# Optimization experiments

Measured on AMD Instinct MI355X. Metric: run time of the kernel, lower is better.

The kernel has to match this reference:

```python
import jax, jax.numpy as jnp
import numpy as np
from itertools import product as _prod

B = 2          # batch size
NPB = 4096     # voxels per batch
C = 384        # input_dim
H = 8          # num_heads
OUT = 32       # output_dim (seg classes)
SPATIAL = (32, 256, 256)
POOL_R = np.array([1, 2, 2, 2])    # [1]+query_gs_ratio
COMP_R = np.array([1, 16, 16, 16])  # [1]+compress_ratio


def _coords():
    rng = np.random.default_rng(0)
    rows = []
    for b in range(B):
        cand = np.stack([rng.integers(0, s, 4 * NPB) for s in SPATIAL], 1)
        cand = np.unique(cand, axis=0)
        sel = cand[rng.permutation(len(cand))[:NPB]]
        rows.append(np.concatenate([np.full((NPB, 1), b, np.int64), sel], 1))
    return np.concatenate(rows).astype(np.int32)


def setup_inputs() -> dict:
    idx = _coords()                     # [N,4] unique (b,z,y,x)
    N = idx.shape[0]
    pool_u, pool_inv = np.unique(idx // POOL_R, axis=0, return_inverse=True)
    emb_u, emb_inv = np.unique(idx // COMP_R, axis=0, return_inverse=True)
    # submanifold 3x3x3 neighbor table (same batch), -1 = missing
    lut = {tuple(r): i for i, r in enumerate(idx.tolist())}
    nbr = np.full((N, 27), -1, np.int32)
    rows = idx.tolist()
    for k, (dz, dy, dx) in enumerate(_prod((-1, 0, 1), repeat=3)):
        for i, (b, z, y, x) in enumerate(rows):
            nbr[i, k] = lut.get((b, z + dz, y + dy, x + dx), -1)
    key = jax.random.key(0)
    ks = jax.random.split(key, 12)
    g = lambda k, shp, s: jax.random.normal(k, shp, jnp.float32) * s
    s = 1.0 / float(np.sqrt(C))
    return dict(
        feats=g(ks[0], (N, C), 1.0),
        W_pool=g(ks[1], (C, C), s), b_pool=jnp.zeros((C,), jnp.float32),
        W_emb=g(ks[2], (C, C), s), b_emb=jnp.zeros((C,), jnp.float32),
        Wq=g(ks[3], (C, C), s), bq=jnp.zeros((C,), jnp.float32),
        Wk=g(ks[4], (C, C), s), bk=jnp.zeros((C,), jnp.float32),
        Wv=g(ks[5], (C, C), s), bv=jnp.zeros((C,), jnp.float32),
        Wo=g(ks[6], (C, C), s), bo=jnp.zeros((C,), jnp.float32),
        W_conv=g(ks[7], (27, C, OUT), 1.0 / float(np.sqrt(27 * C))),
        b_conv=jnp.zeros((OUT,), jnp.float32),
        pool_inv=jnp.asarray(pool_inv, jnp.int32),
        pool_coords=jnp.asarray(pool_u, jnp.int32),
        emb_inv=jnp.asarray(emb_inv, jnp.int32),
        emb_coords=jnp.asarray(emb_u, jnp.int32),
        nbr_idx=jnp.asarray(nbr),
        batch_size=B,
    )


def _sine_pe(xyz, d_pos):
    # xyz: [n,3] normalized to [0,1]; PositionEmbeddingCoordsSine (3detr-style)
    cdim = d_pos // xyz.shape[1]
    dim_t = 10000.0 ** (2.0 * (jnp.arange(cdim) // 2).astype(jnp.float32) / cdim)
    emb = (xyz * (2.0 * jnp.pi))[:, :, None] / dim_t          # [n,3,cdim]
    pe = jnp.stack([jnp.sin(emb[..., 0::2]), jnp.cos(emb[..., 1::2])], -1)
    return pe.reshape(xyz.shape[0], -1)                        # [n,d_pos]


def reference(feats, W_pool, b_pool, W_emb, b_emb, Wq, bq, Wk, bk, Wv, bv,
              Wo, bo, W_conv, b_conv, pool_inv, pool_coords, emb_inv,
              emb_coords, nbr_idx, batch_size):
    Mp, Me, Cc = pool_coords.shape[0], emb_coords.shape[0], feats.shape[1]
    hd = Cc // H
    # query path: linear + scatter_max over pool cells
    pool_f = jax.ops.segment_max(feats @ W_pool + b_pool, pool_inv, num_segments=Mp)
    # kv path: linear + scatter_max over compressed cells (coords of argmax rows
    # within a cell all equal the unique cell coord, so mean == unique coord)
    emb_f = jax.ops.segment_max(feats @ W_emb + b_emb, emb_inv, num_segments=Me)
    # per-batch min/max-normalized sine positional encoding on concat(emb,pool)
    emb_xyz = emb_coords[:, 1:].astype(jnp.float32)
    pool_xyz = pool_coords[:, 1:].astype(jnp.float32)
    all_xyz = jnp.concatenate([emb_xyz, pool_xyz], 0)
    bids = jnp.concatenate([emb_coords[:, 0], pool_coords[:, 0]], 0)
    mins = jax.ops.segment_min(all_xyz, bids, num_segments=batch_size)
    maxs = jax.ops.segment_max(all_xyz, bids, num_segments=batch_size)
    norm = (all_xyz - mins[bids]) / (maxs[bids] - mins[bids] + 1e-6)
    pe = _sine_pe(norm, Cc)
    emb_f = emb_f + pe[:Me]
    pool_f = pool_f + pe[Me:]
    # multi-head cross-attention, masked to same-batch pairs
    q = (pool_f @ Wq + bq).reshape(Mp, H, hd)
    k = (emb_f @ Wk + bk).reshape(Me, H, hd)
    v = (emb_f @ Wv + bv).reshape(Me, H, hd)
    scores = jnp.einsum('phd,ehd->hpe', q, k) / jnp.sqrt(jnp.float32(hd))
    same_b = pool_coords[:, 0][None, :, None] == emb_coords[:, 0][None, None, :]
    attn = jax.nn.softmax(jnp.where(same_b, scores, -1e9), axis=-1)
    o = jnp.einsum('hpe,ehd->phd', attn, v).reshape(Mp, Cc) @ Wo + bo
    # broadcast back to voxels + residual
    new_f = feats + o[pool_inv]
    # SubMConv3d seg head: gather 27 neighbors, contract with kernel
    valid = (nbr_idx >= 0)[:, :, None]
    gathered = jnp.where(valid, new_f[jnp.maximum(nbr_idx, 0)], 0.0)  # [N,27,C]
    logits = jnp.einsum('nkc,kco->no', gathered, W_conv) + b_conv
    return logits
```

## Files before the change

kernel.cpp:

```cpp
#include <hip/hip_runtime.h>
#include <hip/hip_bf16.h>
#include <math.h>

#define CDIM 384
#define NHEAD 8
#define HD 48
#define OUTD 32
#define MAXB 16
#define CONVK 10368

typedef __bf16 bf16x8 __attribute__((ext_vector_type(8)));
typedef float f32x4 __attribute__((ext_vector_type(4)));

__device__ __forceinline__ f32x4 mfma16(bf16x8 a, bf16x8 b, f32x4 c) {
  return __builtin_amdgcn_mfma_f32_16x16x32_bf16(a, b, c, 0, 0, 0);
}
__device__ __forceinline__ bf16x8 zero8() {
  bf16x8 z = {(__bf16)0.f, (__bf16)0.f, (__bf16)0.f, (__bf16)0.f,
              (__bf16)0.f, (__bf16)0.f, (__bf16)0.f, (__bf16)0.f};
  return z;
}

__device__ __forceinline__ unsigned enc_f(float f) {
  unsigned u = __float_as_uint(f);
  return (u & 0x80000000u) ? ~u : (u | 0x80000000u);
}
__device__ __forceinline__ float dec_f(unsigned u) {
  unsigned v = (u & 0x80000000u) ? (u ^ 0x80000000u) : ~u;
  return __uint_as_float(v);
}

__global__ void init_small_kernel(int* smin, int* smax, int* eb) {
  int t = threadIdx.x;
  if (t < MAXB * 3) { smin[t] = 0x7fffffff; smax[t] = (int)0x80000000; }
  if (t <= MAXB) eb[t] = 0;
}

__global__ void minmax_kernel(const int* __restrict__ ec, int Me,
                              const int* __restrict__ pc, int Mp,
                              int* smin, int* smax) {
  __shared__ int lmin[MAXB * 3], lmax[MAXB * 3];
  int t = threadIdx.x;
  if (t < MAXB * 3) { lmin[t] = 0x7fffffff; lmax[t] = (int)0x80000000; }
  __syncthreads();
  int i = blockIdx.x * blockDim.x + t;
  int tot = Me + Mp;
  if (i < tot) {
    const int* r = (i < Me) ? (ec + 4 * i) : (pc + 4 * (i - Me));
    int b = r[0];
    #pragma unroll
    for (int d = 0; d < 3; ++d) {
      atomicMin(&lmin[b * 3 + d], r[1 + d]);
      atomicMax(&lmax[b * 3 + d], r[1 + d]);
    }
  }
  __syncthreads();
  if (t < MAXB * 3) {
    if (lmin[t] != 0x7fffffff) atomicMin(&smin[t], lmin[t]);
    if (lmax[t] != (int)0x80000000) atomicMax(&smax[t], lmax[t]);
  }
}

__global__ void ebound_kernel(const int* __restrict__ ec, int Me,
                              const int* __restrict__ bsz, int* eb) {
  int e = blockIdx.x * blockDim.x + threadIdx.x;
  if (e == 0) { eb[0] = 0; eb[bsz[0]] = Me; }
  if (e > 0 && e < Me) {
    int b0 = ec[4 * (e - 1)], b1 = ec[4 * e];
    for (int bb = b0 + 1; bb <= b1; ++bb) eb[bb] = e;
  }
}

__global__ __launch_bounds__(256) void prep_kernel(
    const float* __restrict__ feats, __hip_bfloat16* __restrict__ feats16, int N,
    const float* __restrict__ W_pool, const float* __restrict__ W_emb,
    const float* __restrict__ Wk, const float* __restrict__ Wv,
    const float* __restrict__ Wq, const float* __restrict__ Wo,
    __hip_bfloat16* __restrict__ Wt_pe, __hip_bfloat16* __restrict__ Wt_kv,
    __hip_bfloat16* __restrict__ Wt_q, __hip_bfloat16* __restrict__ Wt_o,
    const float* __restrict__ Wc, __hip_bfloat16* __restrict__ Wct,
    __hip_bfloat16* __restrict__ vt, int Mepad,
    int nbF, int nbW, int nbC) {
  int b = blockIdx.x;
  int t = threadIdx.x;
  if (b < nbF) {
    int v = b * 256 + t;
    if (v < N * 48) {
      float4 a0 = *reinterpret_cast<const float4*>(feats + (size_t)v * 8);
      float4 a1 = *reinterpret_cast<const float4*>(feats + (size_t)v * 8 + 4);
      __hip_bfloat16 tmp[8] = {
        __float2bfloat16(a0.x), __float2bfloat16(a0.y), __float2bfloat16(a0.z), __float2bfloat16(a0.w),
        __float2bfloat16(a1.x), __float2bfloat16(a1.y), __float2bfloat16(a1.z), __float2bfloat16(a1.w)};
      *reinterpret_cast<bf16x8*>(feats16 + (size_t)v * 8) = *reinterpret_cast<const bf16x8*>(tmp);
    }
    return;
  }
  b -= nbF;
  if (b < 6 * nbW) {
    int m = b / nbW;
    int v = (b - m * nbW) * 256 + t;
    if (v >= CDIM * 48) return;
    const float* src;
    __hip_bfloat16* dst;
    switch (m) {
      case 0: src = W_pool; dst = Wt_pe; break;
      case 1: src = W_emb;  dst = Wt_pe + (size_t)CDIM * CDIM; break;
      case 2: src = Wk;     dst = Wt_kv; break;
      case 3: src = Wv;     dst = Wt_kv + (size_t)CDIM * CDIM; break;
      case 4: src = Wq;     dst = Wt_q; break;
      default: src = Wo;    dst = Wt_o; break;
    }
    int n = v / 48, k8 = (v - n * 48) * 8;
    __hip_bfloat16 tmp[8];
    #pragma unroll
    for (int u = 0; u < 8; ++u) tmp[u] = __float2bfloat16(src[(size_t)(k8 + u) * CDIM + n]);
    *reinterpret_cast<bf16x8*>(dst + (size_t)n * CDIM + k8) = *reinterpret_cast<const bf16x8*>(tmp);
    return;
  }
  b -= 6 * nbW;
  if (b < nbC) {
    int v = b * 256 + t;
    if (v >= OUTD * (CONVK / 8)) return;
    int n = v / (CONVK / 8), k8 = (v - n * (CONVK / 8)) * 8;
    __hip_bfloat16 tmp[8];
    #pragma unroll
    for (int u = 0; u < 8; ++u) tmp[u] = __float2bfloat16(Wc[(size_t)(k8 + u) * OUTD + n]);
    *reinterpret_cast<bf16x8*>(Wct + (size_t)n * CONVK + k8) = *reinterpret_cast<const bf16x8*>(tmp);
    return;
  }
  b -= nbC;
  {
    int v = b * 256 + t;
    if (v < NHEAD * Mepad) {
      int h = v / Mepad, e = v - h * Mepad;
      vt[(size_t)(h * 64 + HD) * Mepad + e] = __float2bfloat16(1.0f);
    }
  }
}

__global__ void pe_kernel(const unsigned* __restrict__ encP, const unsigned* __restrict__ encE,
                          __hip_bfloat16* __restrict__ pool16, __hip_bfloat16* __restrict__ emb16,
                          const int* __restrict__ pc, int Mp,
                          const int* __restrict__ ec, int Me,
                          const int* __restrict__ smin, const int* __restrict__ smax) {
  int gid = blockIdx.x * blockDim.x + threadIdx.x;
  int total = (Mp + Me) * CDIM;
  if (gid >= total) return;
  int row = gid / CDIM, c = gid - row * CDIM;
  const int* coords;
  const unsigned* src;
  __hip_bfloat16* dst;
  int lrow;
  if (row < Me) { lrow = row; coords = ec + 4 * row; src = encE; dst = emb16; }
  else { lrow = row - Me; coords = pc + 4 * lrow; src = encP; dst = pool16; }
  int b = coords[0];
  int dim = c >> 7;
  int i = c & 127;
  int j = i >> 1;
  float x = (float)coords[1 + dim];
  float mn = (float)smin[b * 3 + dim];
  float mx = (float)smax[b * 3 + dim];
  float nrm = (x - mn) / (mx - mn + 1e-6f);
  float freq = exp2f(-(float)j * 0.20762050593046014f);
  float arg = nrm * 6.283185307179586f * freq;
  float pe = (i & 1) ? cosf(arg) : sinf(arg);
  float val = dec_f(src[(size_t)lrow * CDIM + c]) + pe;
  dst[(size_t)lrow * CDIM + c] = __float2bfloat16(val);
}

template <int EPI>
__global__ __launch_bounds__(256) void mgemm_kernel(
    const __hip_bfloat16* __restrict__ A, int M,
    const __hip_bfloat16* __restrict__ Wt,
    const float* __restrict__ bias0, const float* __restrict__ bias1,
    void* __restrict__ d0, void* __restrict__ d1,
    const int* __restrict__ inv0, const int* __restrict__ inv1,
    int Mepad) {
  __shared__ __align__(16) __hip_bfloat16 As[128][72];
  __shared__ __align__(16) __hip_bfloat16 Bs[64][72];
  const int m0 = blockIdx.x * 128;
  const int n0 = blockIdx.y * 64;
  const int t = threadIdx.x;
  const int lane = t & 63, w = t >> 6;
  const int wr = w >> 1, wc = w & 1;
  const int lq = lane & 15, lg = lane >> 4;

  f32x4 acc[4][2];
  #pragma unroll
  for (int i = 0; i < 4; ++i) {
    acc[i][0] = (f32x4){0.f, 0.f, 0.f, 0.f};
    acc[i][1] = (f32x4){0.f, 0.f, 0.f, 0.f};
  }
  const int arow = t >> 3;
  const int acol = (t & 7) * 8;

  for (int k0 = 0; k0 < CDIM; k0 += 64) {
    #pragma unroll
    for (int i = 0; i < 4; ++i) {
      int r = arow + i * 32;
      int gr = m0 + r;
      bf16x8 val = zero8();
      if (gr < M) val = *reinterpret_cast<const bf16x8*>(A + (size_t)gr * CDIM + k0 + acol);
      *reinterpret_cast<bf16x8*>(&As[r][acol]) = val;
    }
    #pragma unroll
    for (int i = 0; i < 2; ++i) {
      int r = arow + i * 32;
      bf16x8 val = *reinterpret_cast<const bf16x8*>(Wt + (size_t)(n0 + r) * CDIM + k0 + acol);
      *reinterpret_cast<bf16x8*>(&Bs[r][acol]) = val;
    }
    __syncthreads();
    #pragma unroll
    for (int ks = 0; ks < 2; ++ks) {
      bf16x8 af[4], bfv[2];
      #pragma unroll
      for (int fm = 0; fm < 4; ++fm)
        af[fm] = *reinterpret_cast<const bf16x8*>(&As[wr * 64 + fm * 16 + lq][ks * 32 + lg * 8]);
      #pragma unroll
      for (int fn = 0; fn < 2; ++fn)
        bfv[fn] = *reinterpret_cast<const bf16x8*>(&Bs[wc * 32 + fn * 16 + lq][ks * 32 + lg * 8]);
      #pragma unroll
      for (int fm = 0; fm < 4; ++fm)
        #pragma unroll
        for (int fn = 0; fn < 2; ++fn)
          acc[fm][fn] = mfma16(af[fm], bfv[fn], acc[fm][fn]);
    }
    __syncthreads();
  }

  const bool sec = (n0 >= CDIM);
  const int nb = n0 - (sec ? CDIM : 0) + wc * 32;
  const int nA = nb + lq, nB = nb + 16 + lq;

  if (EPI == 0) {
    const float* bias = sec ? bias1 : bias0;
    unsigned* dst = (unsigned*)(sec ? d1 : d0);
    const int* inv = sec ? inv1 : inv0;
    float bA = bias[nA], bB = bias[nB];
    #pragma unroll
    for (int fm = 0; fm < 4; ++fm)
      #pragma unroll
      for (int j = 0; j < 4; ++j) {
        int r = m0 + wr * 64 + fm * 16 + lg * 4 + j;
        if (r < M) {
          int seg = inv[r];
          atomicMax(&dst[(size_t)seg * CDIM + nA], enc_f(acc[fm][0][j] + bA));
          atomicMax(&dst[(size_t)seg * CDIM + nB], enc_f(acc[fm][1][j] + bB));
        }
      }
  } else if (EPI == 1) {
    float bA = bias0[nA], bB = bias0[nB];
    float* dst = (float*)d0;
    #pragma unroll
    for (int fm = 0; fm < 4; ++fm)
      #pragma unroll
      for (int j = 0; j < 4; ++j) {
        int r = m0 + wr * 64 + fm * 16 + lg * 4 + j;
        if (r < M) {
          dst[(size_t)r * CDIM + nA] = acc[fm][0][j] + bA;
          dst[(size_t)r * CDIM + nB] = acc[fm][1][j] + bB;
        }
      }
  } else if (EPI == 2) {
    const float scale = 0.14433756729740643f;
    float bA = bias0[nA], bB = bias0[nB];
    int hA = nA / HD, dA = nA - hA * HD;
    int hB = nB / HD, dB = nB - hB * HD;
    __hip_bfloat16* dst = (__hip_bfloat16*)d0;
    #pragma unroll
    for (int fm = 0; fm < 4; ++fm)
      #pragma unroll
      for (int j = 0; j < 4; ++j) {
        int r = m0 + wr * 64 + fm * 16 + lg * 4 + j;
        if (r < M) {
          dst[(size_t)r * 512 + hA * 64 + dA] = __float2bfloat16((acc[fm][0][j] + bA) * scale);
          dst[(size_t)r * 512 + hB * 64 + dB] = __float2bfloat16((acc[fm][1][j] + bB) * scale);
        }
      }
  } else {
    if (!sec) {
      float bA = bias0[nA], bB = bias0[nB];
      int hA = nA / HD, dA = nA - hA * HD;
      int hB = nB / HD, dB = nB - hB * HD;
      __hip_bfloat16* dst = (__hip_bfloat16*)d0;
      #pragma unroll
      for (int fm = 0; fm < 4; ++fm)
        #pragma unroll
        for (int j = 0; j < 4; ++j) {
          int r = m0 + wr * 64 + fm * 16 + lg * 4 + j;
          if (r < M) {
            dst[(size_t)r * 512 + hA * 64 + dA] = __float2bfloat16(acc[fm][0][j] + bA);
            dst[(size_t)r * 512 + hB * 64 + dB] = __float2bfloat16(acc[fm][1][j] + bB);
          }
        }
    } else {
      float bA = bias1[nA], bB = bias1[nB];
      int hA = nA / HD, dA = nA - hA * HD;
      int hB = nB / HD, dB = nB - hB * HD;
      __hip_bfloat16* dst = (__hip_bfloat16*)d1;
      #pragma unroll
      for (int fm = 0; fm < 4; ++fm)
        #pragma unroll
        for (int j = 0; j < 4; ++j) {
          int r = m0 + wr * 64 + fm * 16 + lg * 4 + j;
          if (r < M) {
            dst[(size_t)(hA * 64 + dA) * Mepad + r] = __float2bfloat16(acc[fm][0][j] + bA);
            dst[(size_t)(hB * 64 + dB) * Mepad + r] = __float2bfloat16(acc[fm][1][j] + bB);
          }
        }
    }
  }
}

__global__ __launch_bounds__(256) void attn_mfma_kernel(
    const __hip_bfloat16* __restrict__ qb, const __hip_bfloat16* __restrict__ kb,
    const __hip_bfloat16* __restrict__ vt, int Mepad,
    const int* __restrict__ pc, const int* __restrict__ eb,
    int Mp, int Me, __hip_bfloat16* __restrict__ ob) {
  __shared__ __align__(16) __hip_bfloat16 Ks[64][72];
  __shared__ __align__(16) __hip_bfloat16 Vs[64][72];
  __shared__ __align__(16) __hip_bfloat16 pl[4][16][72];
  __shared__ int s_lo[4], s_hi[4];
  const int h = blockIdx.y;
  const int t = threadIdx.x;
  const int wv = t >> 6, lane = t & 63;
  const int lq = lane & 15, lg = lane >> 4;
  const int q0 = blockIdx.x * 64 + wv * 16;

  int lo[4], hi[4];
  #pragma unroll
  for (int r = 0; r < 4; ++r) {
    int q = q0 + lg * 4 + r;
    if (q < Mp) { int b = pc[4 * q]; lo[r] = eb[b]; hi[r] = eb[b + 1]; }
    else { lo[r] = 0x7fffffff; hi[r] = 0; }
  }
  int wlo = min(min(lo[0], lo[1]), min(lo[2], lo[3]));
  int whi = max(max(hi[0], hi[1]), max(hi[2], hi[3]));
  #pragma unroll
  for (int off = 1; off < 64; off <<= 1) {
    wlo = min(wlo, __shfl_xor(wlo, off));
    whi = max(whi, __shfl_xor(whi, off));
  }
  if (lane == 0) { s_lo[wv] = wlo; s_hi[wv] = whi; }
  __syncthreads();
  int blo = min(min(s_lo[0], s_lo[1]), min(s_lo[2], s_lo[3]));
  int bhi = max(max(s_hi[0], s_hi[1]), max(s_hi[2], s_hi[3]));
  blo &= ~63;

  int qrow = min(q0 + lq, Mp - 1);
  const __hip_bfloat16* qp = qb + (size_t)qrow * 512 + h * 64 + lg * 8;
  bf16x8 aq0 = *reinterpret_cast<const bf16x8*>(qp);
  bf16x8 aq1 = *reinterpret_cast<const bf16x8*>(qp + 32);

  const int str = t >> 2;
  const int stc = (t & 3) * 16;
  const __hip_bfloat16* vrow = vt + (size_t)(h * 64 + str) * Mepad + stc;

  f32x4 zero = {0.f, 0.f, 0.f, 0.f};
  f32x4 oacc[4];
  oacc[0] = zero; oacc[1] = zero; oacc[2] = zero; oacc[3] = zero;

  bf16x8 k0, k1, v0, v1;
  auto load_tile = [&](int e0) {
    int er = e0 + str;
    k0 = zero8(); k1 = zero8();
    if (er < Me) {
      const __hip_bfloat16* kp = kb + (size_t)er * 512 + h * 64 + stc;
      k0 = *reinterpret_cast<const bf16x8*>(kp);
      k1 = *reinterpret_cast<const bf16x8*>(kp + 8);
    }
    v0 = *reinterpret_cast<const bf16x8*>(vrow + e0);
    v1 = *reinterpret_cast<const bf16x8*>(vrow + e0 + 8);
  };
  load_tile(blo);

  for (int e0 = blo; e0 < bhi; e0 += 64) {
    __syncthreads();
    *reinterpret_cast<bf16x8*>(&Ks[str][stc]) = k0;
    *reinterpret_cast<bf16x8*>(&Ks[str][stc + 8]) = k1;
    *reinterpret_cast<bf16x8*>(&Vs[str][stc]) = v0;
    *reinterpret_cast<bf16x8*>(&Vs[str][stc + 8]) = v1;
    __syncthreads();
    if (e0 + 64 < bhi) load_tile(e0 + 64);

    f32x4 sf[4];
    #pragma unroll
    for (int s = 0; s < 4; ++s) {
      bf16x8 bk0 = *reinterpret_cast<const bf16x8*>(&Ks[s * 16 + lq][lg * 8]);
      bf16x8 bk1 = *reinterpret_cast<const bf16x8*>(&Ks[s * 16 + lq][32 + lg * 8]);
      f32x4 z = zero;
      z = mfma16(aq0, bk0, z);
      z = mfma16(aq1, bk1, z);
      sf[s] = z;
    }
    #pragma unroll
    for (int s = 0; s < 4; ++s) {
      int e = e0 + s * 16 + lq;
      #pragma unroll
      for (int r = 0; r < 4; ++r) {
        bool m = (e >= lo[r]) && (e < hi[r]);
        float p = m ? __expf(sf[s][r]) : 0.f;
        pl[wv][lg * 4 + r][s * 16 + lq] = __float2bfloat16(p);
      }
    }
    asm volatile("s_waitcnt lgkmcnt(0)" ::: "memory");
    __builtin_amdgcn_sched_barrier(0);
    #pragma unroll
    for (int ks = 0; ks < 2; ++ks) {
      bf16x8 ap = *reinterpret_cast<const bf16x8*>(&pl[wv][lq][ks * 32 + lg * 8]);
      #pragma unroll
      for (int dt = 0; dt < 4; ++dt) {
        bf16x8 bv = *reinterpret_cast<const bf16x8*>(&Vs[dt * 16 + lq][ks * 32 + lg * 8]);
        oacc[dt] = mfma16(ap, bv, oacc[dt]);
      }
    }
  }

  #pragma unroll
  for (int r = 0; r < 4; ++r) {
    float l = __shfl(oacc[3][r], (lane & 48));
    int q = q0 + lg * 4 + r;
    if (q < Mp && l > 0.f) {
      float inv = 1.0f / l;
      __hip_bfloat16* op = ob + (size_t)q * CDIM + h * HD;
      op[lq]      = __float2bfloat16(oacc[0][r] * inv);
      op[16 + lq] = __float2bfloat16(oacc[1][r] * inv);
      op[32 + lq] = __float2bfloat16(oacc[2][r] * inv);
    }
  }
}

__global__ void newf16_kernel(const float* __restrict__ feats, const float* __restrict__ o2,
                              const int* __restrict__ pinv, __hip_bfloat16* __restrict__ nf,
                              int N) {
  int v = blockIdx.x * 256 + threadIdx.x;
  if (v >= N * 48) return;
  int n = v / 48, c8 = (v - n * 48) * 8;
  const float* fp = feats + (size_t)n * CDIM + c8;
  const float* op = o2 + (size_t)pinv[n] * CDIM + c8;
  float4 a0 = *reinterpret_cast<const float4*>(fp);
  float4 a1 = *reinterpret_cast<const float4*>(fp + 4);
  float4 b0 = *reinterpret_cast<const float4*>(op);
  float4 b1 = *reinterpret_cast<const float4*>(op + 4);
  __hip_bfloat16 tmp[8] = {
    __float2bfloat16(a0.x + b0.x), __float2bfloat16(a0.y + b0.y),
    __float2bfloat16(a0.z + b0.z), __float2bfloat16(a0.w + b0.w),
    __float2bfloat16(a1.x + b1.x), __float2bfloat16(a1.y + b1.y),
    __float2bfloat16(a1.z + b1.z), __float2bfloat16(a1.w + b1.w)};
  *reinterpret_cast<bf16x8*>(nf + (size_t)v * 8) = *reinterpret_cast<const bf16x8*>(tmp);
}

__global__ __launch_bounds__(256) void mconv_kernel(
    const __hip_bfloat16* __restrict__ nf, const int* __restrict__ nbr,
    const __hip_bfloat16* __restrict__ Wct, float* __restrict__ outp, int N) {
  __shared__ __align__(16) __hip_bfloat16 As[128][72];
  __shared__ __align__(16) __hip_bfloat16 Bs[32][72];
  __shared__ int jrow[128];
  const int n0 = blockIdx.x * 128;
  const int kg = blockIdx.y;
  const int t = threadIdx.x;
  const int lane = t & 63, w = t >> 6;
  const int lq = lane & 15, lg = lane >> 4;
  f32x4 acc[2][2];
  acc[0][0] = (f32x4){0.f,0.f,0.f,0.f}; acc[0][1] = acc[0][0];
  acc[1][0] = acc[0][0]; acc[1][1] = acc[0][0];
  const int arow = t >> 3, acol = (t & 7) * 8;

  for (int kk = kg * 3; kk < kg * 3 + 3; ++kk) {
    __syncthreads();
    if (t < 128) {
      int n = n0 + t;
      jrow[t] = (n < N) ? nbr[(size_t)n * 27 + kk] : -1;
    }
    __syncthreads();
    for (int c0 = 0; c0 < CDIM; c0 += 64) {
      #pragma unroll
      for (int i = 0; i < 4; ++i) {
        int r = arow + i * 32;
        int j = jrow[r];
        bf16x8 val = zero8();
        if (j >= 0) val = *reinterpret_cast<const bf16x8*>(nf + (size_t)j * CDIM + c0 + acol);
        *reinterpret_cast<bf16x8*>(&As[r][acol]) = val;
      }
      {
        int r = t >> 3;
        bf16x8 val = *reinterpret_cast<const bf16x8*>(Wct + (size_t)r * CONVK + kk * CDIM + c0 + acol);
        *reinterpret_cast<bf16x8*>(&Bs[r][acol]) = val;
      }
      __syncthreads();
      #pragma unroll
      for (int ks = 0; ks < 2; ++ks) {
        bf16x8 af[2], bfv[2];
        #pragma unroll
        for (int fm = 0; fm < 2; ++fm)
          af[fm] = *reinterpret_cast<const bf16x8*>(&As[w * 32 + fm * 16 + lq][ks * 32 + lg * 8]);
        #pragma unroll
        for (int fn = 0; fn < 2; ++fn)
          bfv[fn] = *reinterpret_cast<const bf16x8*>(&Bs[fn * 16 + lq][ks * 32 + lg * 8]);
        #pragma unroll
        for (int fm = 0; fm < 2; ++fm)
          #pragma unroll
          for (int fn = 0; fn < 2; ++fn)
            acc[fm][fn] = mfma16(af[fm], bfv[fn], acc[fm][fn]);
      }
      __syncthreads();
    }
  }
  #pragma unroll
  for (int fm = 0; fm < 2; ++fm)
    #pragma unroll
    for (int j = 0; j < 4; ++j) {
      int r = n0 + w * 32 + fm * 16 + lg * 4 + j;
      if (r < N) {
        #pragma unroll
        for (int fn = 0; fn < 2; ++fn)
          outp[((size_t)kg * N + r) * OUTD + fn * 16 + lq] = acc[fm][fn][j];
      }
    }
}

__global__ void conv_reduce_kernel(const float* __restrict__ outp,
                                   const float* __restrict__ bc,
                                   float* __restrict__ out, int N) {
  int v = blockIdx.x * 256 + threadIdx.x;
  if (v >= N * OUTD) return;
  int oo = v & (OUTD - 1);
  float s = bc[oo];
  #pragma unroll
  for (int kg = 0; kg < 9; ++kg) s += outp[(size_t)kg * N * OUTD + v];
  out[v] = s;
}

extern "C" void kernel_launch(void* const* d_in, const int* in_sizes, int n_in,
                              void* d_out, int out_size, void* d_ws, size_t ws_size,
                              hipStream_t stream) {
  const float* feats  = (const float*)d_in[0];
  const float* W_pool = (const float*)d_in[1];
  const float* b_pool = (const float*)d_in[2];
  const float* W_emb  = (const float*)d_in[3];
  const float* b_emb  = (const float*)d_in[4];
  const float* Wq = (const float*)d_in[5];  const float* bq = (const float*)d_in[6];
  const float* Wk = (const float*)d_in[7];  const float* bk = (const float*)d_in[8];
  const float* Wv = (const float*)d_in[9];  const float* bv = (const float*)d_in[10];
  const float* Wo = (const float*)d_in[11]; const float* bo = (const float*)d_in[12];
  const float* Wc = (const float*)d_in[13]; const float* bc = (const float*)d_in[14];
  const int* pool_inv    = (const int*)d_in[15];
  const int* pool_coords = (const int*)d_in[16];
  const int* emb_inv     = (const int*)d_in[17];
  const int* emb_coords  = (const int*)d_in[18];
  const int* nbr         = (const int*)d_in[19];
  const int* bsz         = (const int*)d_in[20];
  int N  = in_sizes[0] / CDIM;
  int Mp = in_sizes[16] / 4;
  int Me = in_sizes[18] / 4;
  int Mepad = ((Me >> 6) + 2) << 6;

  char* wsb = (char*)d_ws;
  size_t off = 0;
  auto alloc = [&](size_t bytes) { void* p = wsb + off; off += (bytes + 255) & ~(size_t)255; return p; };
  unsigned* encA = (unsigned*)alloc((size_t)Mp * CDIM * 4);
  unsigned* encB = (unsigned*)alloc((size_t)Me * CDIM * 4);
  __hip_bfloat16* vt = (__hip_bfloat16*)alloc((size_t)512 * Mepad * 2);
  size_t zspan1 = off;
  __hip_bfloat16* pool16  = (__hip_bfloat16*)alloc((size_t)Mp * CDIM * 2);
  __hip_bfloat16* emb16   = (__hip_bfloat16*)alloc((size_t)Me * CDIM * 2);
  __hip_bfloat16* feats16 = (__hip_bfloat16*)alloc((size_t)N * CDIM * 2);
  float* o2 = (float*)alloc((size_t)Mp * CDIM * 4 > (size_t)9 * N * OUTD * 4
                                ? (size_t)Mp * CDIM * 4 : (size_t)9 * N * OUTD * 4);
  __hip_bfloat16* Wt_pe = (__hip_bfloat16*)alloc((size_t)768 * CDIM * 2);
  __hip_bfloat16* Wt_kv = (__hip_bfloat16*)alloc((size_t)768 * CDIM * 2);
  __hip_bfloat16* Wt_q  = (__hip_bfloat16*)alloc((size_t)CDIM * CDIM * 2);
  __hip_bfloat16* Wt_o  = (__hip_bfloat16*)alloc((size_t)CDIM * CDIM * 2);
  __hip_bfloat16* Wct   = (__hip_bfloat16*)alloc((size_t)OUTD * CONVK * 2);
  int* smin = (int*)alloc(MAXB * 3 * 4);
  int* smax = (int*)alloc(MAXB * 3 * 4);
  int* eb   = (int*)alloc((MAXB + 1) * 4);

  __hip_bfloat16* q16  = (__hip_bfloat16*)encA;
  __hip_bfloat16* k16  = (__hip_bfloat16*)encB;
  __hip_bfloat16* ob16 = pool16;
  __hip_bfloat16* newf16 = feats16;
  float* outp = o2;

  hipMemsetAsync(wsb, 0, zspan1, stream);
  init_small_kernel<<<1, 64, 0, stream>>>(smin, smax, eb);
  {
    int tot = Me + Mp;
    minmax_kernel<<<(tot + 255) / 256, 256, 0, stream>>>(emb_coords, Me, pool_coords, Mp, smin, smax);
    ebound_kernel<<<(Me + 255) / 256, 256, 0, stream>>>(emb_coords, Me, bsz, eb);
  }
  int nbF = (N * 48 + 255) / 256;
  int nbW = (CDIM * 48 + 255) / 256;
  int nbC = (OUTD * (CONVK / 8) + 255) / 256;
  int nbV = (NHEAD * Mepad + 255) / 256;
  prep_kernel<<<nbF + 6 * nbW + nbC + nbV, 256, 0, stream>>>(
      feats, feats16, N, W_pool, W_emb, Wk, Wv, Wq, Wo,
      Wt_pe, Wt_kv, Wt_q, Wt_o, Wc, Wct, vt, Mepad, nbF, nbW, nbC);

  mgemm_kernel<0><<<dim3((N + 127) / 128, 12), 256, 0, stream>>>(
      feats16, N, Wt_pe, b_pool, b_emb, encA, encB, pool_inv, emb_inv, 0);
  pe_kernel<<<((Mp + Me) * CDIM + 255) / 256, 256, 0, stream>>>(
      encA, encB, pool16, emb16, pool_coords, Mp, emb_coords, Me, smin, smax);

  hipMemsetAsync(encA, 0, (size_t)((char*)encB - (char*)encA) + (size_t)Me * 1024, stream);

  mgemm_kernel<2><<<dim3((Mp + 127) / 128, 6), 256, 0, stream>>>(
      pool16, Mp, Wt_q, bq, nullptr, q16, nullptr, nullptr, nullptr, 0);
  mgemm_kernel<3><<<dim3((Me + 127) / 128, 12), 256, 0, stream>>>(
      emb16, Me, Wt_kv, bk, bv, k16, vt, nullptr, nullptr, Mepad);

  attn_mfma_kernel<<<dim3((Mp + 63) / 64, NHEAD), 256, 0, stream>>>(
      q16, k16, vt, Mepad, pool_coords, eb, Mp, Me, ob16);

  mgemm_kernel<1><<<dim3((Mp + 127) / 128, 6), 256, 0, stream>>>(
      ob16, Mp, Wt_o, bo, nullptr, o2, nullptr, nullptr, nullptr, 0);

  newf16_kernel<<<(N * 48 + 255) / 256, 256, 0, stream>>>(feats, o2, pool_inv, newf16, N);

  mconv_kernel<<<dim3((N + 127) / 128, 9), 256, 0, stream>>>(newf16, nbr, Wct, outp, N);
  conv_reduce_kernel<<<(N * OUTD + 255) / 256, 256, 0, stream>>>(outp, bc, (float*)d_out, N);
}
```

Measured before the change: 194.6 us.

## Fuse setup kernels into prep, coalesce transposes, pre-reduce segment-max atomics, skip mask in attention

Folds the min/max and batch-boundary kernels into the prep kernel and replaces the init kernel with memsets, cutting launch count. Changes weight-transpose indexing so adjacent threads read adjacent source columns for coalescing. The pooling epilogue merges consecutive rows with the same segment before issuing atomicMax, and attention folds log2e into the Q scale to use exp2f, skipping mask checks for interior tiles. Correctness relies on memset byte patterns producing the right min/max sentinels and on eb not needing zero init.

```diff
diff --git a/kernel.cpp b/kernel.cpp
--- a/kernel.cpp
+++ b/kernel.cpp
@@ -28,47 +28,6 @@
 __device__ __forceinline__ float dec_f(unsigned u) {
   unsigned v = (u & 0x80000000u) ? (u ^ 0x80000000u) : ~u;
   return __uint_as_float(v);
-}
-
-__global__ void init_small_kernel(int* smin, int* smax, int* eb) {
-  int t = threadIdx.x;
-  if (t < MAXB * 3) { smin[t] = 0x7fffffff; smax[t] = (int)0x80000000; }
-  if (t <= MAXB) eb[t] = 0;
-}
-
-__global__ void minmax_kernel(const int* __restrict__ ec, int Me,
-                              const int* __restrict__ pc, int Mp,
-                              int* smin, int* smax) {
-  __shared__ int lmin[MAXB * 3], lmax[MAXB * 3];
-  int t = threadIdx.x;
-  if (t < MAXB * 3) { lmin[t] = 0x7fffffff; lmax[t] = (int)0x80000000; }
-  __syncthreads();
-  int i = blockIdx.x * blockDim.x + t;
-  int tot = Me + Mp;
-  if (i < tot) {
-    const int* r = (i < Me) ? (ec + 4 * i) : (pc + 4 * (i - Me));
-    int b = r[0];
-    #pragma unroll
-    for (int d = 0; d < 3; ++d) {
-      atomicMin(&lmin[b * 3 + d], r[1 + d]);
-      atomicMax(&lmax[b * 3 + d], r[1 + d]);
-    }
-  }
-  __syncthreads();
-  if (t < MAXB * 3) {
-    if (lmin[t] != 0x7fffffff) atomicMin(&smin[t], lmin[t]);
-    if (lmax[t] != (int)0x80000000) atomicMax(&smax[t], lmax[t]);
-  }
-}
-
-__global__ void ebound_kernel(const int* __restrict__ ec, int Me,
-                              const int* __restrict__ bsz, int* eb) {
-  int e = blockIdx.x * blockDim.x + threadIdx.x;
-  if (e == 0) { eb[0] = 0; eb[bsz[0]] = Me; }
-  if (e > 0 && e < Me) {
-    int b0 = ec[4 * (e - 1)], b1 = ec[4 * e];
-    for (int bb = b0 + 1; bb <= b1; ++bb) eb[bb] = e;
-  }
 }
 
 __global__ __launch_bounds__(256) void prep_kernel(
@@ -80,7 +39,10 @@
     __hip_bfloat16* __restrict__ Wt_q, __hip_bfloat16* __restrict__ Wt_o,
     const float* __restrict__ Wc, __hip_bfloat16* __restrict__ Wct,
     __hip_bfloat16* __restrict__ vt, int Mepad,
-    int nbF, int nbW, int nbC) {
+    const int* __restrict__ ec, const int* __restrict__ pc, int Mp, int Me,
+    const int* __restrict__ bsz, int* smin, int* smax, int* ebv,
+    int nbF, int nbW, int nbC, int nbV, int nbM) {
+  __shared__ int lmin[MAXB * 3], lmax[MAXB * 3];
   int b = blockIdx.x;
   int t = threadIdx.x;
   if (b < nbF) {
@@ -110,7 +72,9 @@
       case 4: src = Wq;     dst = Wt_q; break;
       default: src = Wo;    dst = Wt_o; break;
     }
-    int n = v / 48, k8 = (v - n * 48) * 8;
+    int k8i = v / CDIM;
+    int n = v - k8i * CDIM;
+    int k8 = k8i * 8;
     __hip_bfloat16 tmp[8];
     #pragma unroll
     for (int u = 0; u < 8; ++u) tmp[u] = __float2bfloat16(src[(size_t)(k8 + u) * CDIM + n]);
@@ -121,7 +85,9 @@
   if (b < nbC) {
     int v = b * 256 + t;
     if (v >= OUTD * (CONVK / 8)) return;
-    int n = v / (CONVK / 8), k8 = (v - n * (CONVK / 8)) * 8;
+    int k8i = v >> 5;
+    int n = v & 31;
+    int k8 = k8i * 8;
     __hip_bfloat16 tmp[8];
     #pragma unroll
     for (int u = 0; u < 8; ++u) tmp[u] = __float2bfloat16(Wc[(size_t)(k8 + u) * OUTD + n]);
@@ -129,11 +95,43 @@
     return;
   }
   b -= nbC;
-  {
+  if (b < nbV) {
     int v = b * 256 + t;
     if (v < NHEAD * Mepad) {
       int h = v / Mepad, e = v - h * Mepad;
       vt[(size_t)(h * 64 + HD) * Mepad + e] = __float2bfloat16(1.0f);
+    }
+    return;
+  }
+  b -= nbV;
+  if (b < nbM) {
+    if (t < MAXB * 3) { lmin[t] = 0x7fffffff; lmax[t] = (int)0x80000000; }
+    __syncthreads();
+    int i = b * 256 + t;
+    int tot = Me + Mp;
+    if (i < tot) {
+      const int* r = (i < Me) ? (ec + 4 * i) : (pc + 4 * (i - Me));
+      int bb = r[0];
+      #pragma unroll
+      for (int d = 0; d < 3; ++d) {
+        atomicMin(&lmin[bb * 3 + d], r[1 + d]);
+        atomicMax(&lmax[bb * 3 + d], r[1 + d]);
+      }
+    }
+    __syncthreads();
+    if (t < MAXB * 3) {
+      if (lmin[t] != 0x7fffffff) atomicMin(&smin[t], lmin[t]);
+      if (lmax[t] != (int)0x80000000) atomicMax(&smax[t], lmax[t]);
+    }
+    return;
+  }
+  b -= nbM;
+  {
+    int e = b * 256 + t;
+    if (e == 0) { ebv[0] = 0; ebv[bsz[0]] = Me; }
+    if (e > 0 && e < Me) {
+      int b0 = ec[4 * (e - 1)], b1 = ec[4 * e];
+      for (int bb = b0 + 1; bb <= b1; ++bb) ebv[bb] = e;
     }
   }
 }
@@ -238,16 +236,32 @@
     const int* inv = sec ? inv1 : inv0;
     float bA = bias[nA], bB = bias[nB];
     #pragma unroll
-    for (int fm = 0; fm < 4; ++fm)
+    for (int fm = 0; fm < 4; ++fm) {
+      int rbase = m0 + wr * 64 + fm * 16 + lg * 4;
+      int cs = -1;
+      float mA = 0.f, mB = 0.f;
       #pragma unroll
       for (int j = 0; j < 4; ++j) {
-        int r = m0 + wr * 64 + fm * 16 + lg * 4 + j;
+        int r = rbase + j;
         if (r < M) {
-          int seg = inv[r];
-          atomicMax(&dst[(size_t)seg * CDIM + nA], enc_f(acc[fm][0][j] + bA));
-          atomicMax(&dst[(size_t)seg * CDIM + nB], enc_f(acc[fm][1][j] + bB));
+          int s = inv[r];
+          float vA = acc[fm][0][j] + bA;
+          float vB = acc[fm][1][j] + bB;
+          if (s == cs) { mA = fmaxf(mA, vA); mB = fmaxf(mB, vB); }
+          else {
+            if (cs >= 0) {
+              atomicMax(&dst[(size_t)cs * CDIM + nA], enc_f(mA));
+              atomicMax(&dst[(size_t)cs * CDIM + nB], enc_f(mB));
+            }
+            cs = s; mA = vA; mB = vB;
+          }
         }
       }
+      if (cs >= 0) {
+        atomicMax(&dst[(size_t)cs * CDIM + nA], enc_f(mA));
+        atomicMax(&dst[(size_t)cs * CDIM + nB], enc_f(mB));
+      }
+    }
   } else if (EPI == 1) {
     float bA = bias0[nA], bB = bias0[nB];
     float* dst = (float*)d0;
@@ -262,7 +276,7 @@
         }
       }
   } else if (EPI == 2) {
-    const float scale = 0.14433756729740643f;
+    const float scale = 0.2082350914f;
     float bA = bias0[nA], bB = bias0[nB];
     int hA = nA / HD, dA = nA - hA * HD;
     int hB = nB / HD, dB = nB - hB * HD;
@@ -320,7 +334,7 @@
   __shared__ __align__(16) __hip_bfloat16 Ks[64][72];
   __shared__ __align__(16) __hip_bfloat16 Vs[64][72];
   __shared__ __align__(16) __hip_bfloat16 pl[4][16][72];
-  __shared__ int s_lo[4], s_hi[4];
+  __shared__ int sred[4][4];
   const int h = blockIdx.y;
   const int t = threadIdx.x;
   const int wv = t >> 6, lane = t & 63;
@@ -334,18 +348,26 @@
     if (q < Mp) { int b = pc[4 * q]; lo[r] = eb[b]; hi[r] = eb[b + 1]; }
     else { lo[r] = 0x7fffffff; hi[r] = 0; }
   }
-  int wlo = min(min(lo[0], lo[1]), min(lo[2], lo[3]));
-  int whi = max(max(hi[0], hi[1]), max(hi[2], hi[3]));
+  int lomin = min(min(lo[0], lo[1]), min(lo[2], lo[3]));
+  int lomax = max(max(lo[0], lo[1]), max(lo[2], lo[3]));
+  int himin = min(min(hi[0], hi[1]), min(hi[2], hi[3]));
+  int himax = max(max(hi[0], hi[1]), max(hi[2], hi[3]));
   #pragma unroll
   for (int off = 1; off < 64; off <<= 1) {
-    wlo = min(wlo, __shfl_xor(wlo, off));
-    whi = max(whi, __shfl_xor(whi, off));
-  }
-  if (lane == 0) { s_lo[wv] = wlo; s_hi[wv] = whi; }
+    lomin = min(lomin, __shfl_xor(lomin, off));
+    lomax = max(lomax, __shfl_xor(lomax, off));
+    himin = min(himin, __shfl_xor(himin, off));
+    himax = max(himax, __shfl_xor(himax, off));
+  }
+  if (lane == 0) {
+    sred[wv][0] = lomin; sred[wv][1] = lomax;
+    sred[wv][2] = himin; sred[wv][3] = himax;
+  }
   __syncthreads();
-  int blo = min(min(s_lo[0], s_lo[1]), min(s_lo[2], s_lo[3]));
-  int bhi = max(max(s_hi[0], s_hi[1]), max(s_hi[2], s_hi[3]));
-  blo &= ~63;
+  lomin = min(min(sred[0][0], sred[1][0]), min(sred[2][0], sred[3][0]));
+  lomax = max(max(sred[0][1], sred[1][1]), max(sred[2][1], sred[3][1]));
+  himin = min(min(sred[0][2], sred[1][2]), min(sred[2][2], sred[3][2]));
+  himax = max(max(sred[0][3], sred[1][3]), max(sred[2][3], sred[3][3]));
 
   int qrow = min(q0 + lq, Mp - 1);
   const __hip_bfloat16* qp = qb + (size_t)qrow * 512 + h * 64 + lg * 8;
@@ -372,16 +394,17 @@
     v0 = *reinterpret_cast<const bf16x8*>(vrow + e0);
     v1 = *reinterpret_cast<const bf16x8*>(vrow + e0 + 8);
   };
-  load_tile(blo);
-
-  for (int e0 = blo; e0 < bhi; e0 += 64) {
+  const int e0beg = lomin & ~63;
+  load_tile(e0beg);
+
+  for (int e0 = e0beg; e0 < himax; e0 += 64) {
     __syncthreads();
     *reinterpret_cast<bf16x8*>(&Ks[str][stc]) = k0;
     *reinterpret_cast<bf16x8*>(&Ks[str][stc + 8]) = k1;
     *reinterpret_cast<bf16x8*>(&Vs[str][stc]) = v0;
     *reinterpret_cast<bf16x8*>(&Vs[str][stc + 8]) = v1;
     __syncthreads();
-    if (e0 + 64 < bhi) load_tile(e0 + 64);
+    if (e0 + 64 < himax) load_tile(e0 + 64);
 
     f32x4 sf[4];
     #pragma unroll
@@ -393,14 +416,23 @@
       z = mfma16(aq1, bk1, z);
       sf[s] = z;
     }
-    #pragma unroll
-    for (int s = 0; s < 4; ++s) {
-      int e = e0 + s * 16 + lq;
-      #pragma unroll
-      for (int r = 0; r < 4; ++r) {
-        bool m = (e >= lo[r]) && (e < hi[r]);
-        float p = m ? __expf(sf[s][r]) : 0.f;
-        pl[wv][lg * 4 + r][s * 16 + lq] = __float2bfloat16(p);
+    const bool interior = (e0 >= lomax) && (e0 + 64 <= himin);
+    if (interior) {
+      #pragma unroll
+      for (int s = 0; s < 4; ++s)
+        #pragma unroll
+        for (int r = 0; r < 4; ++r)
+          pl[wv][lg * 4 + r][s * 16 + lq] = __float2bfloat16(exp2f(sf[s][r]));
+    } else {
+      #pragma unroll
+      for (int s = 0; s < 4; ++s) {
+        int e = e0 + s * 16 + lq;
+        #pragma unroll
+        for (int r = 0; r < 4; ++r) {
+          bool m = (e >= lo[r]) && (e < hi[r]);
+          float p = m ? exp2f(sf[s][r]) : 0.f;
+          pl[wv][lg * 4 + r][s * 16 + lq] = __float2bfloat16(p);
+        }
       }
     }
     asm volatile("s_waitcnt lgkmcnt(0)" ::: "memory");
@@ -583,19 +615,20 @@
   float* outp = o2;
 
   hipMemsetAsync(wsb, 0, zspan1, stream);
-  init_small_kernel<<<1, 64, 0, stream>>>(smin, smax, eb);
-  {
-    int tot = Me + Mp;
-    minmax_kernel<<<(tot + 255) / 256, 256, 0, stream>>>(emb_coords, Me, pool_coords, Mp, smin, smax);
-    ebound_kernel<<<(Me + 255) / 256, 256, 0, stream>>>(emb_coords, Me, bsz, eb);
-  }
+  hipMemsetAsync(smin, 0x7f, MAXB * 3 * 4, stream);
+  hipMemsetAsync(smax, 0x80, MAXB * 3 * 4, stream);
+
   int nbF = (N * 48 + 255) / 256;
   int nbW = (CDIM * 48 + 255) / 256;
   int nbC = (OUTD * (CONVK / 8) + 255) / 256;
   int nbV = (NHEAD * Mepad + 255) / 256;
-  prep_kernel<<<nbF + 6 * nbW + nbC + nbV, 256, 0, stream>>>(
+  int nbM = (Mp + Me + 255) / 256;
+  int nbE = (Me + 255) / 256;
+  prep_kernel<<<nbF + 6 * nbW + nbC + nbV + nbM + nbE, 256, 0, stream>>>(
       feats, feats16, N, W_pool, W_emb, Wk, Wv, Wq, Wo,
-      Wt_pe, Wt_kv, Wt_q, Wt_o, Wc, Wct, vt, Mepad, nbF, nbW, nbC);
+      Wt_pe, Wt_kv, Wt_q, Wt_o, Wc, Wct, vt, Mepad,
+      emb_coords, pool_coords, Mp, Me, bsz, smin, smax, eb,
+      nbF, nbW, nbC, nbV, nbM);
 
   mgemm_kernel<0><<<dim3((N + 127) / 128, 12), 256, 0, stream>>>(
       feats16, N, Wt_pe, b_pool, b_emb, encA, encB, pool_inv, emb_inv, 0);
```

After: 192.5 us. No clear change (-1.1%).
